# Kernel optimization log

Measured on AMD Instinct MI355X. Metric: run time of the kernel, lower is better.

## Reference

```python
import jax, jax.numpy as jnp
import numpy as np

B, S, E = 2, 2048, 2048
H, D = 16, 128  # num_heads, head_dim = E // H


def setup_inputs() -> dict:
    key = jax.random.key(0)
    ks = jax.random.split(key, 5)
    hidden_states = jax.random.normal(ks[0], (B, S, E), dtype=jnp.float32) * 0.02
    wq = jax.random.normal(ks[1], (E, E), dtype=jnp.float32) * 0.02
    wk = jax.random.normal(ks[2], (E, E), dtype=jnp.float32) * 0.02
    wv = jax.random.normal(ks[3], (E, E), dtype=jnp.float32) * 0.02
    wo = jax.random.normal(ks[4], (E, E), dtype=jnp.float32) * 0.02
    bo = jnp.zeros((E,), dtype=jnp.float32)
    return {"hidden_states": hidden_states, "wq": wq, "wk": wk, "wv": wv, "wo": wo, "bo": bo}


def _split_heads(x):
    # [B, S, E] -> [B, H, S, D]
    return x.reshape(B, S, H, D).transpose(0, 2, 1, 3)


def reference(hidden_states, wq, wk, wv, wo, bo):
    q = _split_heads(hidden_states @ wq)  # [B,H,S,D]
    k = _split_heads(hidden_states @ wk)
    v = _split_heads(hidden_states @ wv)

    # GPT-Neo: no 1/sqrt(d) scaling; scores computed in fp32
    attn_weights = jnp.einsum("bhqd,bhkd->bhqk", q.astype(jnp.float32), k.astype(jnp.float32))

    causal_mask = jnp.tril(jnp.ones((S, S), dtype=bool))  # bias[:, :, :S, :S]
    # Faithful quirk: masked positions get the GLOBAL MIN of attn_weights, not -inf
    mask_value = jnp.min(attn_weights)
    attn_weights = jnp.where(causal_mask, attn_weights, mask_value)

    attn_weights = jax.nn.softmax(attn_weights, axis=-1).astype(v.dtype)
    attn_output = jnp.einsum("bhqk,bhkd->bhqd", attn_weights, v)  # [B,H,S,D]

    # merge heads: [B,H,S,D] -> [B,S,E]
    attn_output = attn_output.transpose(0, 2, 1, 3).reshape(B, S, E)
    attn_output = attn_output @ wo + bo
    return attn_output
```

## Files before the change

### kernel.cpp

```cpp
#include <hip/hip_runtime.h>

typedef unsigned short u16;
typedef unsigned int   u32;
typedef __attribute__((ext_vector_type(4))) float f32x4;
typedef __attribute__((ext_vector_type(4))) u32   u32x4;
typedef __attribute__((ext_vector_type(8))) __bf16 bf16x8;

#define S_LEN 2048
#define EMB   2048
#define NH    16
#define HD    128
#define NBH   32
#define MTOT  4096
#define NUP   120
#define NBMIN (NBH * NUP + 512)

__device__ __forceinline__ u16 f2bf(float f) {
    u32 u = __float_as_uint(f);
    return (u16)((u + 0x7FFFu + ((u >> 16) & 1u)) >> 16);
}
__device__ __forceinline__ float bf2f(u16 v) {
    return __uint_as_float(((u32)v) << 16);
}
__device__ __forceinline__ bf16x8 ld_frag(const u16* p) {
    return __builtin_bit_cast(bf16x8, *(const u32x4*)p);
}
__device__ __forceinline__ void gld_lds16(const void* g, void* l) {
    __builtin_amdgcn_global_load_lds(
        (__attribute__((address_space(1))) void*)(g),
        (__attribute__((address_space(3))) void*)(l), 16, 0, 0);
}

__global__ __launch_bounds__(256) void cast_x_kernel(
    const float* __restrict__ X, u16* __restrict__ Xb)
{
    const size_t i = ((size_t)blockIdx.x * 256 + threadIdx.x) * 8;
    float4 a = *(const float4*)&X[i];
    float4 b = *(const float4*)&X[i + 4];
    u32x4 o;
    o.x = (u32)f2bf(a.x) | ((u32)f2bf(a.y) << 16);
    o.y = (u32)f2bf(a.z) | ((u32)f2bf(a.w) << 16);
    o.z = (u32)f2bf(b.x) | ((u32)f2bf(b.y) << 16);
    o.w = (u32)f2bf(b.z) | ((u32)f2bf(b.w) << 16);
    *(u32x4*)&Xb[i] = o;
}

__global__ __launch_bounds__(256) void transpose_cast_w_kernel(
    const float* __restrict__ W0, const float* __restrict__ W1,
    const float* __restrict__ W2, const float* __restrict__ W3,
    u16* __restrict__ T0, u16* __restrict__ T1,
    u16* __restrict__ T2, u16* __restrict__ T3)
{
    __shared__ float Ls[64][68];
    const int t = threadIdx.x;
    const int n0 = blockIdx.x * 64, k0 = blockIdx.y * 64;
    const int z = blockIdx.z;
    const float* __restrict__ W = (z == 0) ? W0 : (z == 1) ? W1 : (z == 2) ? W2 : W3;
    u16* __restrict__ T = (z == 0) ? T0 : (z == 1) ? T1 : (z == 2) ? T2 : T3;

#pragma unroll
    for (int p = 0; p < 4; ++p) {
        const int r = (t >> 4) + 16 * p;
        const int c = (t & 15) * 4;
        *(float4*)&Ls[r][c] = *(const float4*)&W[(size_t)(k0 + r) * EMB + n0 + c];
    }
    __syncthreads();
    const int nl = t >> 2, q = t & 3;
    u32 pk[8];
#pragma unroll
    for (int j = 0; j < 8; ++j) {
        u16 lo = f2bf(Ls[q * 16 + 2 * j][nl]);
        u16 hi = f2bf(Ls[q * 16 + 2 * j + 1][nl]);
        pk[j] = (u32)lo | ((u32)hi << 16);
    }
    u32x4 o0 = {pk[0], pk[1], pk[2], pk[3]};
    u32x4 o1 = {pk[4], pk[5], pk[6], pk[7]};
    u16* dst = &T[(size_t)(n0 + nl) * EMB + k0 + q * 16];
    *(u32x4*)&dst[0] = o0;
    *(u32x4*)&dst[8] = o1;
}

__global__ __launch_bounds__(256) void transpose_v_kernel(
    const u16* __restrict__ V, u16* __restrict__ Vt)
{
    __shared__ u16 Ls[64][72];
    const int t = threadIdx.x;
    const int s0 = blockIdx.x * 64, d0 = blockIdx.y * 64, bh = blockIdx.z;
    const u16* __restrict__ src0 = V + ((size_t)bh * S_LEN) * HD;
    {
        const int r = t >> 2, c0 = (t & 3) * 16;
        const u16* src = &src0[(size_t)(s0 + r) * HD + d0 + c0];
        *(u32x4*)&Ls[r][c0]     = *(const u32x4*)&src[0];
        *(u32x4*)&Ls[r][c0 + 8] = *(const u32x4*)&src[8];
    }
    __syncthreads();
    const int dl = t >> 2, q = t & 3;
    u32 pk[8];
#pragma unroll
    for (int j = 0; j < 8; ++j) {
        u16 lo = Ls[q * 16 + 2 * j][dl];
        u16 hi = Ls[q * 16 + 2 * j + 1][dl];
        pk[j] = (u32)lo | ((u32)hi << 16);
    }
    u32x4 o0 = {pk[0], pk[1], pk[2], pk[3]};
    u32x4 o1 = {pk[4], pk[5], pk[6], pk[7]};
    u16* dst = &Vt[((size_t)bh * HD + d0 + dl) * S_LEN + s0 + q * 16];
    *(u32x4*)&dst[0] = o0;
    *(u32x4*)&dst[8] = o1;
}

__global__ __launch_bounds__(256) void gemm_qkv_mfma(
    const u16* __restrict__ Xb,
    const u16* __restrict__ Wtq, const u16* __restrict__ Wtk,
    const u16* __restrict__ Wtv,
    u16* __restrict__ Qo, u16* __restrict__ Ko, u16* __restrict__ Vo)
{
    __shared__ __attribute__((aligned(16))) u16 As[128 * 32];
    __shared__ __attribute__((aligned(16))) u16 Bs[128 * 32];
    const int t = threadIdx.x;
    const int w = t >> 6, lane = t & 63;
    const int wy = w >> 1, wx = w & 1;
    const int n0 = blockIdx.x * 128, m0 = blockIdx.y * 128;
    const int z = blockIdx.z;
    const u16* __restrict__ Wt = (z == 0) ? Wtq : (z == 1) ? Wtk : Wtv;
    u16* __restrict__ O = (z == 0) ? Qo : (z == 1) ? Ko : Vo;

    const int srow = lane >> 2, scol = (lane & 3) * 8;
    const u16* Ag = &Xb[(size_t)(m0 + w * 32 + srow) * EMB + scol];
    const u16* Bg = &Wt[(size_t)(n0 + w * 32 + srow) * EMB + scol];
    u16* Al0 = &As[(w * 32) * 32];
    u16* Al1 = &As[(w * 32 + 16) * 32];
    u16* Bl0 = &Bs[(w * 32) * 32];
    u16* Bl1 = &Bs[(w * 32 + 16) * 32];

    const int fm = lane & 15, fk = (lane >> 4) * 8;
    f32x4 acc[4][4];
#pragma unroll
    for (int i = 0; i < 4; ++i)
#pragma unroll
        for (int j = 0; j < 4; ++j) acc[i][j] = (f32x4)0.0f;

    for (int k0 = 0; k0 < EMB; k0 += 32) {
        __syncthreads();
        gld_lds16(Ag + k0, Al0);
        gld_lds16(Ag + 16 * EMB + k0, Al1);
        gld_lds16(Bg + k0, Bl0);
        gld_lds16(Bg + 16 * EMB + k0, Bl1);
        __syncthreads();
        bf16x8 af[4], bfr[4];
#pragma unroll
        for (int mi = 0; mi < 4; ++mi)
            af[mi] = ld_frag(&As[(64 * wy + 16 * mi + fm) * 32 + fk]);
#pragma unroll
        for (int ni = 0; ni < 4; ++ni)
            bfr[ni] = ld_frag(&Bs[(64 * wx + 16 * ni + fm) * 32 + fk]);
#pragma unroll
        for (int mi = 0; mi < 4; ++mi)
#pragma unroll
            for (int ni = 0; ni < 4; ++ni)
                acc[mi][ni] = __builtin_amdgcn_mfma_f32_16x16x32_bf16(
                    af[mi], bfr[ni], acc[mi][ni], 0, 0, 0);
    }

    const int q4 = (lane >> 4) * 4;
#pragma unroll
    for (int mi = 0; mi < 4; ++mi)
#pragma unroll
        for (int ni = 0; ni < 4; ++ni) {
            const int n = n0 + 64 * wx + 16 * ni + (lane & 15);
            const int h = n >> 7, d = n & 127;
#pragma unroll
            for (int r = 0; r < 4; ++r) {
                const int m = m0 + 64 * wy + 16 * mi + q4 + r;
                const int bb = m >> 11, s = m & 2047;
                O[(((size_t)(bb * NH + h) * S_LEN) + s) * HD + d] = f2bf(acc[mi][ni][r]);
            }
        }
}

__global__ __launch_bounds__(256) void gemm_out_mfma(
    const u16* __restrict__ Ab, const u16* __restrict__ Wto,
    const float* __restrict__ bias, float* __restrict__ Out)
{
    __shared__ __attribute__((aligned(16))) u16 As[128 * 32];
    __shared__ __attribute__((aligned(16))) u16 Bs[128 * 32];
    const int t = threadIdx.x;
    const int w = t >> 6, lane = t & 63;
    const int wy = w >> 1, wx = w & 1;
    const int n0 = blockIdx.x * 128, m0 = blockIdx.y * 128;

    const int srow = lane >> 2, scol = (lane & 3) * 8;
    const u16* Ag = &Ab[(size_t)(m0 + w * 32 + srow) * EMB + scol];
    const u16* Bg = &Wto[(size_t)(n0 + w * 32 + srow) * EMB + scol];
    u16* Al0 = &As[(w * 32) * 32];
    u16* Al1 = &As[(w * 32 + 16) * 32];
    u16* Bl0 = &Bs[(w * 32) * 32];
    u16* Bl1 = &Bs[(w * 32 + 16) * 32];

    const int fm = lane & 15, fk = (lane >> 4) * 8;
    f32x4 acc[4][4];
#pragma unroll
    for (int i = 0; i < 4; ++i)
#pragma unroll
        for (int j = 0; j < 4; ++j) acc[i][j] = (f32x4)0.0f;

    for (int k0 = 0; k0 < EMB; k0 += 32) {
        __syncthreads();
        gld_lds16(Ag + k0, Al0);
        gld_lds16(Ag + 16 * EMB + k0, Al1);
        gld_lds16(Bg + k0, Bl0);
        gld_lds16(Bg + 16 * EMB + k0, Bl1);
        __syncthreads();
        bf16x8 af[4], bfr[4];
#pragma unroll
        for (int mi = 0; mi < 4; ++mi)
            af[mi] = ld_frag(&As[(64 * wy + 16 * mi + fm) * 32 + fk]);
#pragma unroll
        for (int ni = 0; ni < 4; ++ni)
            bfr[ni] = ld_frag(&Bs[(64 * wx + 16 * ni + fm) * 32 + fk]);
#pragma unroll
        for (int mi = 0; mi < 4; ++mi)
#pragma unroll
            for (int ni = 0; ni < 4; ++ni)
                acc[mi][ni] = __builtin_amdgcn_mfma_f32_16x16x32_bf16(
                    af[mi], bfr[ni], acc[mi][ni], 0, 0, 0);
    }

    const int q4 = (lane >> 4) * 4;
#pragma unroll
    for (int mi = 0; mi < 4; ++mi)
#pragma unroll
        for (int ni = 0; ni < 4; ++ni) {
            const int n = n0 + 64 * wx + 16 * ni + (lane & 15);
            const float bv = bias[n];
#pragma unroll
            for (int r = 0; r < 4; ++r) {
                const int m = m0 + 64 * wy + 16 * mi + q4 + r;
                Out[(size_t)m * EMB + n] = acc[mi][ni][r] + bv;
            }
        }
}

__global__ __launch_bounds__(256) void qk_upper_min(
    const u16* __restrict__ Q, const u16* __restrict__ K,
    float* __restrict__ blockmin)
{
    __shared__ __attribute__((aligned(16))) u16 As[128 * 32];
    __shared__ __attribute__((aligned(16))) u16 Bs[128 * 32];
    __shared__ float sm[256];
    const int t = threadIdx.x;
    const int w = t >> 6, lane = t & 63;
    const int wy = w >> 1, wx = w & 1;
    int u = blockIdx.x, qt = 0, cnt = 15;
    while (u >= cnt) { u -= cnt; ++qt; cnt = 15 - qt; }
    const int kt = qt + 1 + u;
    const int bh = blockIdx.y;

    const int srow = lane >> 2, scol = (lane & 3) * 8;
    const u16* Ag = &Q[((size_t)bh * S_LEN + qt * 128 + w * 32 + srow) * HD + scol];
    const u16* Bg = &K[((size_t)bh * S_LEN + kt * 128 + w * 32 + srow) * HD + scol];
    u16* Al0 = &As[(w * 32) * 32];
    u16* Al1 = &As[(w * 32 + 16) * 32];
    u16* Bl0 = &Bs[(w * 32) * 32];
    u16* Bl1 = &Bs[(w * 32 + 16) * 32];

    const int fm = lane & 15, fk = (lane >> 4) * 8;
    f32x4 acc[4][4];
#pragma unroll
    for (int i = 0; i < 4; ++i)
#pragma unroll
        for (int j = 0; j < 4; ++j) acc[i][j] = (f32x4)0.0f;

    for (int k0 = 0; k0 < HD; k0 += 32) {
        __syncthreads();
        gld_lds16(Ag + k0, Al0);
        gld_lds16(Ag + 16 * HD + k0, Al1);
        gld_lds16(Bg + k0, Bl0);
        gld_lds16(Bg + 16 * HD + k0, Bl1);
        __syncthreads();
        bf16x8 af[4], bfr[4];
#pragma unroll
        for (int mi = 0; mi < 4; ++mi)
            af[mi] = ld_frag(&As[(64 * wy + 16 * mi + fm) * 32 + fk]);
#pragma unroll
        for (int ni = 0; ni < 4; ++ni)
            bfr[ni] = ld_frag(&Bs[(64 * wx + 16 * ni + fm) * 32 + fk]);
#pragma unroll
        for (int mi = 0; mi < 4; ++mi)
#pragma unroll
            for (int ni = 0; ni < 4; ++ni)
                acc[mi][ni] = __builtin_amdgcn_mfma_f32_16x16x32_bf16(
                    af[mi], bfr[ni], acc[mi][ni], 0, 0, 0);
    }

    float mn = acc[0][0][0];
#pragma unroll
    for (int mi = 0; mi < 4; ++mi)
#pragma unroll
        for (int ni = 0; ni < 4; ++ni)
#pragma unroll
            for (int r = 0; r < 4; ++r) mn = fminf(mn, acc[mi][ni][r]);
    sm[t] = mn;
    __syncthreads();
    for (int sft = 128; sft > 0; sft >>= 1) {
        if (t < sft) sm[t] = fminf(sm[t], sm[t + sft]);
        __syncthreads();
    }
    if (t == 0) blockmin[(size_t)bh * NUP + blockIdx.x] = sm[0];
}

__global__ __launch_bounds__(256) void reduce_min_kernel(
    const float* __restrict__ bm, float* __restrict__ minval)
{
    __shared__ float sm[256];
    const int t = threadIdx.x;
    float m = 3.0e38f;
    for (int i = t; i < NBMIN; i += 256) m = fminf(m, bm[i]);
    sm[t] = m;
    __syncthreads();
    for (int sft = 128; sft > 0; sft >>= 1) {
        if (t < sft) sm[t] = fminf(sm[t], sm[t + sft]);
        __syncthreads();
    }
    if (t == 0) minval[0] = sm[0];
}

__global__ __launch_bounds__(128) void vchunk_sum_kernel(
    const u16* __restrict__ V, float* __restrict__ csum)
{
    const int chunk = blockIdx.x, bh = blockIdx.y, d = threadIdx.x;
    const u16* vb = V + ((size_t)bh * S_LEN + chunk * 64) * HD + d;
    float s = 0.0f;
    for (int r = 0; r < 64; ++r) s += bf2f(vb[(size_t)r * HD]);
    csum[((size_t)bh * 32 + chunk) * HD + d] = s;
}

__global__ __launch_bounds__(128) void vchunk_suffix_kernel(
    const float* __restrict__ csum, float* __restrict__ csuf)
{
    const int bh = blockIdx.x, d = threadIdx.x;
    float run = 0.0f;
    for (int c = 31; c >= 0; --c) {
        const size_t idx = ((size_t)bh * 32 + c) * HD + d;
        csuf[idx] = run;
        run += csum[idx];
    }
}

__global__ __launch_bounds__(128) void vsuffix_kernel(
    const u16* __restrict__ V, const float* __restrict__ csuf,
    float* __restrict__ vsuf)
{
    const int chunk = blockIdx.x, bh = blockIdx.y, d = threadIdx.x;
    float run = csuf[((size_t)bh * 32 + chunk) * HD + d];
    const size_t base = ((size_t)bh * S_LEN + chunk * 64) * HD + d;
    for (int r = 63; r >= 0; --r) {
        vsuf[base + (size_t)r * HD] = run;
        run += bf2f(V[base + (size_t)r * HD]);
    }
}

__global__ __launch_bounds__(256) void attn_mfma(
    const u16* __restrict__ Q, const u16* __restrict__ K,
    const u16* __restrict__ Vt,
    u16* __restrict__ pacc0, u16* __restrict__ pacc1,
    float* __restrict__ den_p, float* __restrict__ blockmin)
{
    __shared__ __attribute__((aligned(16))) u16 Qs[128 * 136];
    __shared__ __attribute__((aligned(16))) u16 Ps[128 * 136];
    __shared__ __attribute__((aligned(16))) u16 Cs[128 * 32];
    __shared__ float den_l[2][128];
    __shared__ float smn[256];

    const int t = threadIdx.x;
    const int w = t >> 6, lane = t & 63;
    const int wy = w >> 1, wx = w & 1;
    const int pp = blockIdx.x >> 1, hpar = blockIdx.x & 1;
    const int bh = blockIdx.y;
    const int b = bh >> 4, h = bh & 15;

    const u16* __restrict__ Kg  = K + (size_t)bh * S_LEN * HD;
    const u16* __restrict__ Vtg = Vt + (size_t)bh * HD * S_LEN;
    u16* __restrict__ pacc = hpar ? pacc1 : pacc0;

    const int srow = lane >> 2, scol = (lane & 3) * 8;
    const int fm = lane & 15, fk = (lane >> 4) * 8;
    const int q4 = (lane >> 4) * 4;

    float mn = 3.0e38f;

    for (int pass = 0; pass < 2; ++pass) {
        const int qt = pass ? (15 - pp) : pp;
        const int i0 = qt * 128;
        const u16* __restrict__ Qg = Q + ((size_t)bh * S_LEN + i0) * HD;

        __syncthreads();
        {
            const int r = t >> 1, ch = (t & 1) * 64;
            const u16* src = &Qg[(size_t)r * HD + ch];
            u16* dst = &Qs[r * 136 + ch];
#pragma unroll
            for (int j = 0; j < 8; ++j)
                *(u32x4*)&dst[j * 8] = *(const u32x4*)&src[j * 8];
        }

        f32x4 oacc[4][4];
#pragma unroll
        for (int i = 0; i < 4; ++i)
#pragma unroll
            for (int j = 0; j < 4; ++j) oacc[i][j] = (f32x4)0.0f;
        float den[4][4] = {};

        for (int jt = hpar; jt <= qt; jt += 2) {
            const int j0 = jt * 128;
            f32x4 sacc[4][4];
#pragma unroll
            for (int i = 0; i < 4; ++i)
#pragma unroll
                for (int j = 0; j < 4; ++j) sacc[i][j] = (f32x4)0.0f;
            for (int dk = 0; dk < 4; ++dk) {
                __syncthreads();
                {
                    const u16* g = &Kg[(size_t)(j0 + w * 32 + srow) * HD + dk * 32 + scol];
                    gld_lds16(g, &Cs[(w * 32) * 32]);
                    gld_lds16(g + 16 * HD, &Cs[(w * 32 + 16) * 32]);
                }
                __syncthreads();
                bf16x8 af[4], bfr[4];
#pragma unroll
                for (int mi = 0; mi < 4; ++mi)
                    af[mi] = ld_frag(&Qs[(64 * wy + 16 * mi + fm) * 136 + dk * 32 + fk]);
#pragma unroll
                for (int ni = 0; ni < 4; ++ni)
                    bfr[ni] = ld_frag(&Cs[(64 * wx + 16 * ni + fm) * 32 + fk]);
#pragma unroll
                for (int mi = 0; mi < 4; ++mi)
#pragma unroll
                    for (int ni = 0; ni < 4; ++ni)
                        sacc[mi][ni] = __builtin_amdgcn_mfma_f32_16x16x32_bf16(
                            af[mi], bfr[ni], sacc[mi][ni], 0, 0, 0);
            }
            const bool dg = (jt == qt);
#pragma unroll
            for (int mi = 0; mi < 4; ++mi) {
                const int rbase = 64 * wy + 16 * mi + q4;
#pragma unroll
                for (int ni = 0; ni < 4; ++ni) {
                    const int cl = 64 * wx + 16 * ni + (lane & 15);
                    const int jg = j0 + cl;
#pragma unroll
                    for (int r = 0; r < 4; ++r) {
                        const float s = sacc[mi][ni][r];
                        mn = fminf(mn, s);
                        float e = __expf(s);
                        if (dg && jg > i0 + rbase + r) e = 0.0f;
                        den[mi][r] += e;
                        Ps[(rbase + r) * 136 + cl] = f2bf(e);
                    }
                }
            }
            __syncthreads();

            for (int sk = 0; sk < 4; ++sk) {
                if (sk) __syncthreads();
                {
                    const u16* g = &Vtg[(size_t)(w * 32 + srow) * S_LEN + j0 + sk * 32 + scol];
                    gld_lds16(g, &Cs[(w * 32) * 32]);
                    gld_lds16(g + 16 * S_LEN, &Cs[(w * 32 + 16) * 32]);
                }
                __syncthreads();
                bf16x8 pa[4], pb[4];
#pragma unroll
                for (int mi = 0; mi < 4; ++mi)
                    pa[mi] = ld_frag(&Ps[(64 * wy + 16 * mi + fm) * 136 + sk * 32 + fk]);
#pragma unroll
                for (int ni = 0; ni < 4; ++ni)
                    pb[ni] = ld_frag(&Cs[(64 * wx + 16 * ni + fm) * 32 + fk]);
#pragma unroll
                for (int mi = 0; mi < 4; ++mi)
#pragma unroll
                    for (int ni = 0; ni < 4; ++ni)
                        oacc[mi][ni] = __builtin_amdgcn_mfma_f32_16x16x32_bf16(
                            pa[mi], pb[ni], oacc[mi][ni], 0, 0, 0);
            }
        }

#pragma unroll
        for (int mi = 0; mi < 4; ++mi)
#pragma unroll
            for (int r = 0; r < 4; ++r) {
                float v = den[mi][r];
                v += __shfl_xor(v, 1, 64);
                v += __shfl_xor(v, 2, 64);
                v += __shfl_xor(v, 4, 64);
                v += __shfl_xor(v, 8, 64);
                den[mi][r] = v;
            }
        __syncthreads();
        if ((lane & 15) == 0) {
#pragma unroll
            for (int mi = 0; mi < 4; ++mi)
#pragma unroll
                for (int r = 0; r < 4; ++r)
                    den_l[wx][64 * wy + 16 * mi + q4 + r] = den[mi][r];
        }
        __syncthreads();
        if (t < 128)
            den_p[((size_t)hpar * NBH + bh) * S_LEN + i0 + t] =
                den_l[0][t] + den_l[1][t];

#pragma unroll
        for (int mi = 0; mi < 4; ++mi)
#pragma unroll
            for (int ni = 0; ni < 4; ++ni) {
                const int d = 64 * wx + 16 * ni + (lane & 15);
#pragma unroll
                for (int r = 0; r < 4; ++r) {
                    const int row = 64 * wy + 16 * mi + q4 + r;
                    pacc[((size_t)b * S_LEN + i0 + row) * EMB + h * HD + d] =
                        f2bf(oacc[mi][ni][r]);
                }
            }
    }

    __syncthreads();
    smn[t] = mn;
    __syncthreads();
    for (int sft = 128; sft > 0; sft >>= 1) {
        if (t < sft) smn[t] = fminf(smn[t], smn[t + sft]);
        __syncthreads();
    }
    if (t == 0) blockmin[blockIdx.y * 16 + blockIdx.x] = smn[0];
}

__global__ __launch_bounds__(256) void finalize_kernel(
    u16* __restrict__ outm, const u16* __restrict__ pacc1,
    const float* __restrict__ vsuf, const float* __restrict__ den_p,
    const float* __restrict__ minval)
{
    const size_t i = ((size_t)blockIdx.x * 256 + threadIdx.x) * 8;
    const int e = (int)(i & (EMB - 1));
    const int m = (int)(i / EMB);
    const int b = m >> 11, s = m & 2047;
    const int hh = e >> 7, d = e & 127;
    const int bh = b * NH + hh;
    const float em = __expf(minval[0]);
    const float den = den_p[(size_t)bh * S_LEN + s]
                    + den_p[((size_t)NBH + bh) * S_LEN + s]
                    + (float)(S_LEN - 1 - s) * em;
    const float inv = 1.0f / den;
    u32x4 a = *(const u32x4*)&outm[i];
    u32x4 c = *(const u32x4*)&pacc1[i];
    const u16* pa = (const u16*)&a;
    const u16* pc = (const u16*)&c;
    const float* vs = &vsuf[((size_t)bh * S_LEN + s) * HD + d];
    u16 ov[8];
#pragma unroll
    for (int j = 0; j < 8; ++j) {
        const float v = bf2f(pa[j]) + bf2f(pc[j]) + em * vs[j];
        ov[j] = f2bf(v * inv);
    }
    *(u32x4*)&outm[i] = *(const u32x4*)ov;
}

extern "C" void kernel_launch(void* const* d_in, const int* in_sizes, int n_in,
                              void* d_out, int out_size, void* d_ws, size_t ws_size,
                              hipStream_t stream)
{
    (void)in_sizes; (void)n_in; (void)out_size; (void)ws_size;
    const float* hs = (const float*)d_in[0];
    const float* wq = (const float*)d_in[1];
    const float* wk = (const float*)d_in[2];
    const float* wv = (const float*)d_in[3];
    const float* wo = (const float*)d_in[4];
    const float* bo = (const float*)d_in[5];
    float* out = (float*)d_out;

    char* p = (char*)d_ws;
    const size_t TS = (size_t)NBH * S_LEN * HD;
    u16* Xb   = (u16*)p; p += (size_t)MTOT * EMB * 2;
    u16* Wtq  = (u16*)p; p += (size_t)EMB * EMB * 2;
    u16* Wtk  = (u16*)p; p += (size_t)EMB * EMB * 2;
    u16* Wtv  = (u16*)p; p += (size_t)EMB * EMB * 2;
    u16* Wto  = (u16*)p; p += (size_t)EMB * EMB * 2;
    u16* Qb   = (u16*)p; p += TS * 2;
    u16* Kb   = (u16*)p; p += TS * 2;
    u16* Vb   = (u16*)p; p += TS * 2;
    u16* Vtb  = (u16*)p; p += TS * 2;
    u16* outm = (u16*)p; p += (size_t)MTOT * EMB * 2;
    float* vsuf     = (float*)p; p += TS * 4;
    float* csum     = (float*)p; p += (size_t)NBH * 32 * HD * 4;
    float* csuf     = (float*)p; p += (size_t)NBH * 32 * HD * 4;
    float* blockmin = (float*)p; p += 8192 * 4;
    float* minval   = (float*)p; p += 64;
    float* den_p    = (float*)p; p += (size_t)2 * NBH * S_LEN * 4;
    u16* pacc1 = Xb;

    cast_x_kernel<<<4096, 256, 0, stream>>>(hs, Xb);
    transpose_cast_w_kernel<<<dim3(32, 32, 4), 256, 0, stream>>>(
        wq, wk, wv, wo, Wtq, Wtk, Wtv, Wto);

    gemm_qkv_mfma<<<dim3(EMB / 128, MTOT / 128, 3), 256, 0, stream>>>(
        Xb, Wtq, Wtk, Wtv, Qb, Kb, Vb);

    transpose_v_kernel<<<dim3(32, 2, NBH), 256, 0, stream>>>(Vb, Vtb);
    vchunk_sum_kernel<<<dim3(32, NBH), 128, 0, stream>>>(Vb, csum);
    vchunk_suffix_kernel<<<NBH, 128, 0, stream>>>(csum, csuf);
    vsuffix_kernel<<<dim3(32, NBH), 128, 0, stream>>>(Vb, csuf, vsuf);

    qk_upper_min<<<dim3(NUP, NBH), 256, 0, stream>>>(Qb, Kb, blockmin);

    attn_mfma<<<dim3(16, NBH), 256, 0, stream>>>(
        Qb, Kb, Vtb, outm, pacc1, den_p, blockmin + (size_t)NBH * NUP);

    reduce_min_kernel<<<1, 256, 0, stream>>>(blockmin, minval);

    finalize_kernel<<<(MTOT * EMB / 8) / 256, 256, 0, stream>>>(
        outm, pacc1, vsuf, den_p, minval);

    gemm_out_mfma<<<dim3(EMB / 128, MTOT / 128), 256, 0, stream>>>(
        outm, Wto, bo, out);
}
```

Baseline: 494.6 us.

## Fuse upper-triangle QK min into attention kernel with double-buffered K/V loads

Removes the separate qk_upper_min kernel and has attn_mfma compute QK scores for all key tiles, including non-causal ones, only to track the global minimum. K and V tiles now stream through a double-buffered LDS slot so the next tile's load overlaps the current MFMAs. Q fragments are held in registers instead of LDS. The V suffix buffer is stored in bf16 instead of fp32. The aim is to cut a kernel launch, the redundant Q/K reads and the memory traffic, at the cost of higher register pressure and lower precision on the suffix term.

```diff
diff --git a/kernel.cpp b/kernel.cpp
--- a/kernel.cpp
+++ b/kernel.cpp
@@ -12,8 +12,7 @@
 #define HD    128
 #define NBH   32
 #define MTOT  4096
-#define NUP   120
-#define NBMIN (NBH * NUP + 512)
+#define NBMIN 512
 
 __device__ __forceinline__ u16 f2bf(float f) {
     u32 u = __float_as_uint(f);
@@ -241,74 +240,6 @@
         }
 }
 
-__global__ __launch_bounds__(256) void qk_upper_min(
-    const u16* __restrict__ Q, const u16* __restrict__ K,
-    float* __restrict__ blockmin)
-{
-    __shared__ __attribute__((aligned(16))) u16 As[128 * 32];
-    __shared__ __attribute__((aligned(16))) u16 Bs[128 * 32];
-    __shared__ float sm[256];
-    const int t = threadIdx.x;
-    const int w = t >> 6, lane = t & 63;
-    const int wy = w >> 1, wx = w & 1;
-    int u = blockIdx.x, qt = 0, cnt = 15;
-    while (u >= cnt) { u -= cnt; ++qt; cnt = 15 - qt; }
-    const int kt = qt + 1 + u;
-    const int bh = blockIdx.y;
-
-    const int srow = lane >> 2, scol = (lane & 3) * 8;
-    const u16* Ag = &Q[((size_t)bh * S_LEN + qt * 128 + w * 32 + srow) * HD + scol];
-    const u16* Bg = &K[((size_t)bh * S_LEN + kt * 128 + w * 32 + srow) * HD + scol];
-    u16* Al0 = &As[(w * 32) * 32];
-    u16* Al1 = &As[(w * 32 + 16) * 32];
-    u16* Bl0 = &Bs[(w * 32) * 32];
-    u16* Bl1 = &Bs[(w * 32 + 16) * 32];
-
-    const int fm = lane & 15, fk = (lane >> 4) * 8;
-    f32x4 acc[4][4];
-#pragma unroll
-    for (int i = 0; i < 4; ++i)
-#pragma unroll
-        for (int j = 0; j < 4; ++j) acc[i][j] = (f32x4)0.0f;
-
-    for (int k0 = 0; k0 < HD; k0 += 32) {
-        __syncthreads();
-        gld_lds16(Ag + k0, Al0);
-        gld_lds16(Ag + 16 * HD + k0, Al1);
-        gld_lds16(Bg + k0, Bl0);
-        gld_lds16(Bg + 16 * HD + k0, Bl1);
-        __syncthreads();
-        bf16x8 af[4], bfr[4];
-#pragma unroll
-        for (int mi = 0; mi < 4; ++mi)
-            af[mi] = ld_frag(&As[(64 * wy + 16 * mi + fm) * 32 + fk]);
-#pragma unroll
-        for (int ni = 0; ni < 4; ++ni)
-            bfr[ni] = ld_frag(&Bs[(64 * wx + 16 * ni + fm) * 32 + fk]);
-#pragma unroll
-        for (int mi = 0; mi < 4; ++mi)
-#pragma unroll
-            for (int ni = 0; ni < 4; ++ni)
-                acc[mi][ni] = __builtin_amdgcn_mfma_f32_16x16x32_bf16(
-                    af[mi], bfr[ni], acc[mi][ni], 0, 0, 0);
-    }
-
-    float mn = acc[0][0][0];
-#pragma unroll
-    for (int mi = 0; mi < 4; ++mi)
-#pragma unroll
-        for (int ni = 0; ni < 4; ++ni)
-#pragma unroll
-            for (int r = 0; r < 4; ++r) mn = fminf(mn, acc[mi][ni][r]);
-    sm[t] = mn;
-    __syncthreads();
-    for (int sft = 128; sft > 0; sft >>= 1) {
-        if (t < sft) sm[t] = fminf(sm[t], sm[t + sft]);
-        __syncthreads();
-    }
-    if (t == 0) blockmin[(size_t)bh * NUP + blockIdx.x] = sm[0];
-}
-
 __global__ __launch_bounds__(256) void reduce_min_kernel(
     const float* __restrict__ bm, float* __restrict__ minval)
 {
@@ -349,13 +280,13 @@
 
 __global__ __launch_bounds__(128) void vsuffix_kernel(
     const u16* __restrict__ V, const float* __restrict__ csuf,
-    float* __restrict__ vsuf)
+    u16* __restrict__ vsuf)
 {
     const int chunk = blockIdx.x, bh = blockIdx.y, d = threadIdx.x;
     float run = csuf[((size_t)bh * 32 + chunk) * HD + d];
     const size_t base = ((size_t)bh * S_LEN + chunk * 64) * HD + d;
     for (int r = 63; r >= 0; --r) {
-        vsuf[base + (size_t)r * HD] = run;
+        vsuf[base + (size_t)r * HD] = f2bf(run);
         run += bf2f(V[base + (size_t)r * HD]);
     }
 }
@@ -366,9 +297,8 @@
     u16* __restrict__ pacc0, u16* __restrict__ pacc1,
     float* __restrict__ den_p, float* __restrict__ blockmin)
 {
-    __shared__ __attribute__((aligned(16))) u16 Qs[128 * 136];
     __shared__ __attribute__((aligned(16))) u16 Ps[128 * 136];
-    __shared__ __attribute__((aligned(16))) u16 Cs[128 * 32];
+    __shared__ __attribute__((aligned(16))) u16 Cs[2][128 * 32];
     __shared__ float den_l[2][128];
     __shared__ float smn[256];
 
@@ -387,22 +317,33 @@
     const int fm = lane & 15, fk = (lane >> 4) * 8;
     const int q4 = (lane >> 4) * 4;
 
+    u16* cs0a = &Cs[0][(w * 32) * 32];
+    u16* cs0b = &Cs[0][(w * 32 + 16) * 32];
+    u16* cs1a = &Cs[1][(w * 32) * 32];
+    u16* cs1b = &Cs[1][(w * 32 + 16) * 32];
+
     float mn = 3.0e38f;
+    int c = 0;
+
+    {
+        const u16* g = &Kg[(size_t)(hpar * 128 + w * 32 + srow) * HD + scol];
+        gld_lds16(g, cs0a);
+        gld_lds16(g + 16 * HD, cs0b);
+    }
+    __syncthreads();
 
     for (int pass = 0; pass < 2; ++pass) {
         const int qt = pass ? (15 - pp) : pp;
         const int i0 = qt * 128;
         const u16* __restrict__ Qg = Q + ((size_t)bh * S_LEN + i0) * HD;
 
-        __syncthreads();
-        {
-            const int r = t >> 1, ch = (t & 1) * 64;
-            const u16* src = &Qg[(size_t)r * HD + ch];
-            u16* dst = &Qs[r * 136 + ch];
-#pragma unroll
-            for (int j = 0; j < 8; ++j)
-                *(u32x4*)&dst[j * 8] = *(const u32x4*)&src[j * 8];
-        }
+        bf16x8 af[4][4];
+#pragma unroll
+        for (int mi = 0; mi < 4; ++mi)
+#pragma unroll
+            for (int dk = 0; dk < 4; ++dk)
+                af[mi][dk] = ld_frag(
+                    &Qg[(size_t)(64 * wy + 16 * mi + fm) * HD + dk * 32 + fk]);
 
         f32x4 oacc[4][4];
 #pragma unroll
@@ -411,77 +352,114 @@
             for (int j = 0; j < 4; ++j) oacc[i][j] = (f32x4)0.0f;
         float den[4][4] = {};
 
-        for (int jt = hpar; jt <= qt; jt += 2) {
+        for (int ji = 0; ji < 8; ++ji) {
+            const int jt = hpar + 2 * ji;
             const int j0 = jt * 128;
+            const bool causal = (jt <= qt);
+            const bool last_step = (ji == 7);
+            const bool have_next = (!last_step) || (pass == 0);
+            const int nj0 = last_step ? hpar * 128 : (jt + 2) * 128;
+
             f32x4 sacc[4][4];
 #pragma unroll
             for (int i = 0; i < 4; ++i)
 #pragma unroll
                 for (int j = 0; j < 4; ++j) sacc[i][j] = (f32x4)0.0f;
+
             for (int dk = 0; dk < 4; ++dk) {
-                __syncthreads();
-                {
-                    const u16* g = &Kg[(size_t)(j0 + w * 32 + srow) * HD + dk * 32 + scol];
-                    gld_lds16(g, &Cs[(w * 32) * 32]);
-                    gld_lds16(g + 16 * HD, &Cs[(w * 32 + 16) * 32]);
+                u16* na = c ? cs0a : cs1a;
+                u16* nb = c ? cs0b : cs1b;
+                if (dk < 3) {
+                    const u16* g = &Kg[(size_t)(j0 + w * 32 + srow) * HD
+                                       + (dk + 1) * 32 + scol];
+                    gld_lds16(g, na);
+                    gld_lds16(g + 16 * HD, nb);
+                } else if (causal) {
+                    const u16* g = &Vtg[(size_t)(w * 32 + srow) * S_LEN + j0 + scol];
+                    gld_lds16(g, na);
+                    gld_lds16(g + 16 * S_LEN, nb);
+                } else if (have_next) {
+                    const u16* g = &Kg[(size_t)(nj0 + w * 32 + srow) * HD + scol];
+                    gld_lds16(g, na);
+                    gld_lds16(g + 16 * HD, nb);
+                }
+                bf16x8 bfr[4];
+#pragma unroll
+                for (int ni = 0; ni < 4; ++ni)
+                    bfr[ni] = ld_frag(&Cs[c][(64 * wx + 16 * ni + fm) * 32 + fk]);
+#pragma unroll
+                for (int mi = 0; mi < 4; ++mi)
+#pragma unroll
+                    for (int ni = 0; ni < 4; ++ni)
+                        sacc[mi][ni] = __builtin_amdgcn_mfma_f32_16x16x32_bf16(
+                            af[mi][dk], bfr[ni], sacc[mi][ni], 0, 0, 0);
+
+                if (dk == 3) {
+                    if (causal) {
+                        const bool dg = (jt == qt);
+#pragma unroll
+                        for (int mi = 0; mi < 4; ++mi) {
+                            const int rbase = 64 * wy + 16 * mi + q4;
+#pragma unroll
+                            for (int ni = 0; ni < 4; ++ni) {
+                                const int cl = 64 * wx + 16 * ni + fm;
+                                const int jg = j0 + cl;
+#pragma unroll
+                                for (int r = 0; r < 4; ++r) {
+                                    const float s = sacc[mi][ni][r];
+                                    mn = fminf(mn, s);
+                                    float e = __expf(s);
+                                    if (dg && jg > i0 + rbase + r) e = 0.0f;
+                                    den[mi][r] += e;
+                                    Ps[(rbase + r) * 136 + cl] = f2bf(e);
+                                }
+                            }
+                        }
+                    } else {
+#pragma unroll
+                        for (int mi = 0; mi < 4; ++mi)
+#pragma unroll
+                            for (int ni = 0; ni < 4; ++ni)
+#pragma unroll
+                                for (int r = 0; r < 4; ++r)
+                                    mn = fminf(mn, sacc[mi][ni][r]);
+                    }
                 }
                 __syncthreads();
-                bf16x8 af[4], bfr[4];
-#pragma unroll
-                for (int mi = 0; mi < 4; ++mi)
-                    af[mi] = ld_frag(&Qs[(64 * wy + 16 * mi + fm) * 136 + dk * 32 + fk]);
-#pragma unroll
-                for (int ni = 0; ni < 4; ++ni)
-                    bfr[ni] = ld_frag(&Cs[(64 * wx + 16 * ni + fm) * 32 + fk]);
-#pragma unroll
-                for (int mi = 0; mi < 4; ++mi)
+                c ^= 1;
+            }
+
+            if (causal) {
+                for (int sk = 0; sk < 4; ++sk) {
+                    u16* na = c ? cs0a : cs1a;
+                    u16* nb = c ? cs0b : cs1b;
+                    if (sk < 3) {
+                        const u16* g = &Vtg[(size_t)(w * 32 + srow) * S_LEN
+                                            + j0 + (sk + 1) * 32 + scol];
+                        gld_lds16(g, na);
+                        gld_lds16(g + 16 * S_LEN, nb);
+                    } else if (have_next) {
+                        const u16* g = &Kg[(size_t)(nj0 + w * 32 + srow) * HD + scol];
+                        gld_lds16(g, na);
+                        gld_lds16(g + 16 * HD, nb);
+                    }
+                    bf16x8 pa[4], pb[4];
+#pragma unroll
+                    for (int mi = 0; mi < 4; ++mi)
+                        pa[mi] = ld_frag(&Ps[(64 * wy + 16 * mi + fm) * 136
+                                             + sk * 32 + fk]);
 #pragma unroll
                     for (int ni = 0; ni < 4; ++ni)
-                        sacc[mi][ni] = __builtin_amdgcn_mfma_f32_16x16x32_bf16(
-                            af[mi], bfr[ni], sacc[mi][ni], 0, 0, 0);
-            }
-            const bool dg = (jt == qt);
-#pragma unroll
-            for (int mi = 0; mi < 4; ++mi) {
-                const int rbase = 64 * wy + 16 * mi + q4;
-#pragma unroll
-                for (int ni = 0; ni < 4; ++ni) {
-                    const int cl = 64 * wx + 16 * ni + (lane & 15);
-                    const int jg = j0 + cl;
-#pragma unroll
-                    for (int r = 0; r < 4; ++r) {
-                        const float s = sacc[mi][ni][r];
-                        mn = fminf(mn, s);
-                        float e = __expf(s);
-                        if (dg && jg > i0 + rbase + r) e = 0.0f;
-                        den[mi][r] += e;
-                        Ps[(rbase + r) * 136 + cl] = f2bf(e);
-                    }
+                        pb[ni] = ld_frag(&Cs[c][(64 * wx + 16 * ni + fm) * 32 + fk]);
+#pragma unroll
+                    for (int mi = 0; mi < 4; ++mi)
+#pragma unroll
+                        for (int ni = 0; ni < 4; ++ni)
+                            oacc[mi][ni] = __builtin_amdgcn_mfma_f32_16x16x32_bf16(
+                                pa[mi], pb[ni], oacc[mi][ni], 0, 0, 0);
+                    __syncthreads();
+                    c ^= 1;
                 }
-            }
-            __syncthreads();
-
-            for (int sk = 0; sk < 4; ++sk) {
-                if (sk) __syncthreads();
-                {
-                    const u16* g = &Vtg[(size_t)(w * 32 + srow) * S_LEN + j0 + sk * 32 + scol];
-                    gld_lds16(g, &Cs[(w * 32) * 32]);
-                    gld_lds16(g + 16 * S_LEN, &Cs[(w * 32 + 16) * 32]);
-                }
-                __syncthreads();
-                bf16x8 pa[4], pb[4];
-#pragma unroll
-                for (int mi = 0; mi < 4; ++mi)
-                    pa[mi] = ld_frag(&Ps[(64 * wy + 16 * mi + fm) * 136 + sk * 32 + fk]);
-#pragma unroll
-                for (int ni = 0; ni < 4; ++ni)
-                    pb[ni] = ld_frag(&Cs[(64 * wx + 16 * ni + fm) * 32 + fk]);
-#pragma unroll
-                for (int mi = 0; mi < 4; ++mi)
-#pragma unroll
-                    for (int ni = 0; ni < 4; ++ni)
-                        oacc[mi][ni] = __builtin_amdgcn_mfma_f32_16x16x32_bf16(
-                            pa[mi], pb[ni], oacc[mi][ni], 0, 0, 0);
             }
         }
 
@@ -513,7 +491,7 @@
         for (int mi = 0; mi < 4; ++mi)
 #pragma unroll
             for (int ni = 0; ni < 4; ++ni) {
-                const int d = 64 * wx + 16 * ni + (lane & 15);
+                const int d = 64 * wx + 16 * ni + fm;
 #pragma unroll
                 for (int r = 0; r < 4; ++r) {
                     const int row = 64 * wy + 16 * mi + q4 + r;
@@ -521,9 +499,9 @@
                         f2bf(oacc[mi][ni][r]);
                 }
             }
-    }
-
-    __syncthreads();
+        __syncthreads();
+    }
+
     smn[t] = mn;
     __syncthreads();
     for (int sft = 128; sft > 0; sft >>= 1) {
@@ -535,7 +513,7 @@
 
 __global__ __launch_bounds__(256) void finalize_kernel(
     u16* __restrict__ outm, const u16* __restrict__ pacc1,
-    const float* __restrict__ vsuf, const float* __restrict__ den_p,
+    const u16* __restrict__ vsuf, const float* __restrict__ den_p,
     const float* __restrict__ minval)
 {
     const size_t i = ((size_t)blockIdx.x * 256 + threadIdx.x) * 8;
@@ -550,14 +528,15 @@
                     + (float)(S_LEN - 1 - s) * em;
     const float inv = 1.0f / den;
     u32x4 a = *(const u32x4*)&outm[i];
-    u32x4 c = *(const u32x4*)&pacc1[i];
+    u32x4 cc = *(const u32x4*)&pacc1[i];
+    u32x4 vv = *(const u32x4*)&vsuf[((size_t)bh * S_LEN + s) * HD + d];
     const u16* pa = (const u16*)&a;
-    const u16* pc = (const u16*)&c;
-    const float* vs = &vsuf[((size_t)bh * S_LEN + s) * HD + d];
+    const u16* pc = (const u16*)&cc;
+    const u16* pv = (const u16*)&vv;
     u16 ov[8];
 #pragma unroll
     for (int j = 0; j < 8; ++j) {
-        const float v = bf2f(pa[j]) + bf2f(pc[j]) + em * vs[j];
+        const float v = bf2f(pa[j]) + bf2f(pc[j]) + em * bf2f(pv[j]);
         ov[j] = f2bf(v * inv);
     }
     *(u32x4*)&outm[i] = *(const u32x4*)ov;
@@ -588,10 +567,10 @@
     u16* Vb   = (u16*)p; p += TS * 2;
     u16* Vtb  = (u16*)p; p += TS * 2;
     u16* outm = (u16*)p; p += (size_t)MTOT * EMB * 2;
-    float* vsuf     = (float*)p; p += TS * 4;
+    u16* vsuf = (u16*)p; p += TS * 2;
     float* csum     = (float*)p; p += (size_t)NBH * 32 * HD * 4;
     float* csuf     = (float*)p; p += (size_t)NBH * 32 * HD * 4;
-    float* blockmin = (float*)p; p += 8192 * 4;
+    float* blockmin = (float*)p; p += 1024 * 4;
     float* minval   = (float*)p; p += 64;
     float* den_p    = (float*)p; p += (size_t)2 * NBH * S_LEN * 4;
     u16* pacc1 = Xb;
@@ -608,10 +587,8 @@
     vchunk_suffix_kernel<<<NBH, 128, 0, stream>>>(csum, csuf);
     vsuffix_kernel<<<dim3(32, NBH), 128, 0, stream>>>(Vb, csuf, vsuf);
 
-    qk_upper_min<<<dim3(NUP, NBH), 256, 0, stream>>>(Qb, Kb, blockmin);
-
     attn_mfma<<<dim3(16, NBH), 256, 0, stream>>>(
-        Qb, Kb, Vtb, outm, pacc1, den_p, blockmin + (size_t)NBH * NUP);
+        Qb, Kb, Vtb, outm, pacc1, den_p, blockmin);
 
     reduce_min_kernel<<<1, 256, 0, stream>>>(blockmin, minval);
 
```

New measurement: 462.7 us. -6.4%, faster.
